# Kernel optimization log

Measured on AMD Instinct MI355X. Metric: run time of the kernel, lower is better.

Reference implementation:

```python
import jax, jax.numpy as jnp
import numpy as np

B, S, R, A, DW, DR = 64, 32, 128, 64, 512, 512

def setup_inputs() -> dict:
    key = jax.random.key(0)
    ks = jax.random.split(key, 12)
    s = 0.02
    return {
        "b_question_vector": jax.random.normal(ks[0], (B, S, DW), jnp.float32),
        "b_question_mask": jnp.zeros((B, S), dtype=bool),  # True = padding
        "b_r_space": jax.random.randint(ks[1], (B, A), 0, R),
        "b_coverage_t": jax.random.uniform(ks[2], (B, S), jnp.float32),
        "rel_emb": jax.random.normal(ks[3], (R, DR), jnp.float32) * s,
        "Wq": jax.random.normal(ks[4], (DR, DW), jnp.float32) * s,
        "bq": jnp.zeros((DR,), jnp.float32),
        "Wr": jax.random.normal(ks[5], (DR, DR), jnp.float32) * s,
        "br": jnp.zeros((DR,), jnp.float32),
        "Wc": jax.random.normal(ks[6], (DR, 1), jnp.float32) * s,
        "bc": jnp.zeros((DR,), jnp.float32),
        "Watt": jax.random.normal(ks[7], (1, DR), jnp.float32) * s,
        "batt": jnp.zeros((1,), jnp.float32),
    }

def reference(b_question_vector, b_question_mask, b_r_space, b_coverage_t,
              rel_emb, Wq, bq, Wr, br, Wc, bc, Watt, batt):
    # question_linear: [B,S,DW] -> [B,S,DR] (computed once, not repeated R times)
    qp = jnp.einsum('bsw,dw->bsd', b_question_vector, Wq) + bq
    # relation_linear over full embedding table: [R,DR]
    rp = rel_emb @ Wr.T + br
    # coverage_linear: Linear(1, DR) applied to scalar coverage -> [B,S,DR]
    cp = b_coverage_t[:, :, None] * Wc[:, 0] + bc
    # additive attention features, broadcast instead of repeat+view: [B,R,S,DR]
    feat = jnp.tanh(qp[:, None, :, :] + rp[None, :, None, :] + cp[:, None, :, :])
    # W_att: [B,R,S,DR] -> [B,R,S]
    scores = jnp.einsum('brsd,d->brs', feat, Watt[0]) + batt[0]
    scores = jnp.where(b_question_mask[:, None, :], -jnp.inf, scores)
    alpha = jax.nn.softmax(scores, axis=-1)                      # softmax over seq
    ctx = jnp.einsum('brs,bsw->brw', alpha, b_question_vector)   # [B,R,DW]
    # per-batch gather output_i[relation_i] (vectorized)
    out = jnp.take_along_axis(ctx, b_r_space[:, :, None], axis=1)    # [B,A,DW]
    alpha_sel = jnp.take_along_axis(alpha, b_r_space[:, :, None], axis=1)  # [B,A,S]
    return (out, alpha_sel)
```

## Files before the change

kernel.cpp:

```cpp
#include <hip/hip_runtime.h>
#include <hip/hip_bf16.h>
#include <math.h>

#define B_  64
#define S_  32
#define R_  128
#define A_  64
#define DW_ 512
#define DR_ 512

typedef __attribute__((ext_vector_type(8))) short short8;
typedef __attribute__((ext_vector_type(4))) float f32x4;

__device__ __forceinline__ unsigned short bf16_rn(float x) {
    union { float f; unsigned u; } v; v.f = x;
    unsigned r = v.u + 0x7FFF + ((v.u >> 16) & 1);
    return (unsigned short)(r >> 16);
}
__device__ __forceinline__ float bf16_to_f(unsigned short h) {
    union { unsigned u; float f; } v; v.u = ((unsigned)h) << 16;
    return v.f;
}

__device__ __forceinline__ int swz(int row, int chunk) {
    return row * 32 + ((chunk ^ ((row >> 1) & 3)) << 3);
}

__global__ __launch_bounds__(256) void gemm_dual_kernel(
    const float* __restrict__ A0, const float* __restrict__ B0, float* __restrict__ C0,
    int M0, int N0, int K0,
    const float* __restrict__ bias1_0, const float* __restrict__ bias2_0,
    const float* __restrict__ rowv0, const float* __restrict__ colv0,
    const float* __restrict__ A1, const float* __restrict__ B1, float* __restrict__ C1,
    int M1, int N1, int K1,
    const float* __restrict__ bias1_1)
{
    const int z = blockIdx.z;
    const float* Am; const float* Bm; float* C;
    const float *bias1, *bias2, *rowv, *colv;
    int M, N, K;
    if (z == 0) {
        Am = A0; Bm = B0; C = C0; M = M0; N = N0; K = K0;
        bias1 = bias1_0; bias2 = bias2_0; rowv = rowv0; colv = colv0;
    } else {
        Am = A1; Bm = B1; C = C1; M = M1; N = N1; K = K1;
        bias1 = bias1_1; bias2 = nullptr; rowv = nullptr; colv = nullptr;
    }

    const int bm = blockIdx.x * 64;
    const int bn = blockIdx.y * 64;
    if (bm >= M || bn >= N) return;

    __shared__ unsigned short Ahi[2][64 * 32], Alo[2][64 * 32];
    __shared__ unsigned short Bhi[2][64 * 32], Blo[2][64 * 32];

    const int tid  = threadIdx.x;
    const int l    = tid & 63;
    const int w    = tid >> 6;
    const int wr   = w >> 1;
    const int wc   = w & 1;
    const int fr   = l & 15;
    const int fc   = l >> 4;
    const int srow = tid >> 2;
    const int sch  = tid & 3;

    f32x4 acc[2][2] = {};

    float4 ra0, ra1, rb0, rb1;

    {
        const size_t arow = (size_t)(bm + srow) * K + sch * 8;
        const size_t brow = (size_t)(bn + srow) * K + sch * 8;
        ra0 = *(const float4*)&Am[arow];     ra1 = *(const float4*)&Am[arow + 4];
        rb0 = *(const float4*)&Bm[brow];     rb1 = *(const float4*)&Bm[brow + 4];

        short8 ahi, alo, bhi, blo;
        float af[8] = {ra0.x, ra0.y, ra0.z, ra0.w, ra1.x, ra1.y, ra1.z, ra1.w};
        float bf[8] = {rb0.x, rb0.y, rb0.z, rb0.w, rb1.x, rb1.y, rb1.z, rb1.w};
        #pragma unroll
        for (int e = 0; e < 8; ++e) {
            unsigned short h = bf16_rn(af[e]);
            ahi[e] = (short)h;
            alo[e] = (short)bf16_rn(af[e] - bf16_to_f(h));
            unsigned short g = bf16_rn(bf[e]);
            bhi[e] = (short)g;
            blo[e] = (short)bf16_rn(bf[e] - bf16_to_f(g));
        }
        *(short8*)&Ahi[0][swz(srow, sch)] = ahi;
        *(short8*)&Alo[0][swz(srow, sch)] = alo;
        *(short8*)&Bhi[0][swz(srow, sch)] = bhi;
        *(short8*)&Blo[0][swz(srow, sch)] = blo;
    }
    __syncthreads();

    const int nsteps = K >> 5;
    int cur = 0;
    for (int s = 0; s < nsteps; ++s) {
        if (s + 1 < nsteps) {
            const int k0 = (s + 1) << 5;
            const size_t arow = (size_t)(bm + srow) * K + k0 + sch * 8;
            const size_t brow = (size_t)(bn + srow) * K + k0 + sch * 8;
            ra0 = *(const float4*)&Am[arow];     ra1 = *(const float4*)&Am[arow + 4];
            rb0 = *(const float4*)&Bm[brow];     rb1 = *(const float4*)&Bm[brow + 4];
        }

        short8 fahi[2], falo[2], fbhi[2], fblo[2];
        #pragma unroll
        for (int i = 0; i < 2; ++i) {
            const int r = wr * 32 + i * 16 + fr;
            fahi[i] = *(const short8*)&Ahi[cur][swz(r, fc)];
            falo[i] = *(const short8*)&Alo[cur][swz(r, fc)];
            const int c = wc * 32 + i * 16 + fr;
            fbhi[i] = *(const short8*)&Bhi[cur][swz(c, fc)];
            fblo[i] = *(const short8*)&Blo[cur][swz(c, fc)];
        }
        #pragma unroll
        for (int i = 0; i < 2; ++i)
            #pragma unroll
            for (int j = 0; j < 2; ++j) {
                acc[i][j] = __builtin_amdgcn_mfma_f32_16x16x32_bf16(fahi[i], fbhi[j], acc[i][j], 0, 0, 0);
                acc[i][j] = __builtin_amdgcn_mfma_f32_16x16x32_bf16(fahi[i], fblo[j], acc[i][j], 0, 0, 0);
                acc[i][j] = __builtin_amdgcn_mfma_f32_16x16x32_bf16(falo[i], fbhi[j], acc[i][j], 0, 0, 0);
            }

        if (s + 1 < nsteps) {
            short8 ahi, alo, bhi, blo;
            float af[8] = {ra0.x, ra0.y, ra0.z, ra0.w, ra1.x, ra1.y, ra1.z, ra1.w};
            float bf[8] = {rb0.x, rb0.y, rb0.z, rb0.w, rb1.x, rb1.y, rb1.z, rb1.w};
            #pragma unroll
            for (int e = 0; e < 8; ++e) {
                unsigned short h = bf16_rn(af[e]);
                ahi[e] = (short)h;
                alo[e] = (short)bf16_rn(af[e] - bf16_to_f(h));
                unsigned short g = bf16_rn(bf[e]);
                bhi[e] = (short)g;
                blo[e] = (short)bf16_rn(bf[e] - bf16_to_f(g));
            }
            const int nxt = cur ^ 1;
            *(short8*)&Ahi[nxt][swz(srow, sch)] = ahi;
            *(short8*)&Alo[nxt][swz(srow, sch)] = alo;
            *(short8*)&Bhi[nxt][swz(srow, sch)] = bhi;
            *(short8*)&Blo[nxt][swz(srow, sch)] = blo;
            __syncthreads();
            cur = nxt;
        }
    }

    #pragma unroll
    for (int i = 0; i < 2; ++i)
        #pragma unroll
        for (int j = 0; j < 2; ++j) {
            const int n  = bn + wc * 32 + j * 16 + fr;
            const float b1 = bias1[n];
            const float b2 = bias2 ? bias2[n] : 0.0f;
            const float cv = colv ? colv[n] : 0.0f;
            #pragma unroll
            for (int reg = 0; reg < 4; ++reg) {
                const int m = bm + wr * 32 + i * 16 + fc * 4 + reg;
                float v = acc[i][j][reg] + b1 + b2;
                if (rowv) v += rowv[m] * cv;
                C[(size_t)m * N + n] = v;
            }
        }
}

__global__ __launch_bounds__(256) void attn_kernel(
    const float* __restrict__ u,
    const float* __restrict__ rp,
    const float* __restrict__ watt,
    const float* __restrict__ battp,
    const float* __restrict__ qv,
    const unsigned char* __restrict__ mask,
    const int* __restrict__ rspace,
    float* __restrict__ out,
    float* __restrict__ alpha_out)
{
    const int blk  = blockIdx.x;
    const int b    = blk >> 3;
    const int ba0  = b * A_ + ((blk & 7) << 3);
    const int tid  = threadIdx.x;
    const int lane = tid & 63;
    const int wave = tid >> 6;

    const float K2 = 2.8853900817779268f;

    __shared__ float s_scores[8][S_];
    __shared__ float s_alpha[8][S_];

    float wav[8], rp2[8][8];
    {
        const float4* wa4 = (const float4*)watt;
        #pragma unroll
        for (int v = 0; v < 2; ++v) {
            float4 w = wa4[v * 64 + lane];
            wav[v*4+0] = w.x; wav[v*4+1] = w.y; wav[v*4+2] = w.z; wav[v*4+3] = w.w;
        }
        #pragma unroll
        for (int g = 0; g < 8; ++g) {
            const float4* rp4 = (const float4*)(rp + (size_t)rspace[ba0 + g] * DR_);
            #pragma unroll
            for (int v = 0; v < 2; ++v) {
                float4 t = rp4[v * 64 + lane];
                rp2[g][v*4+0] = t.x * K2; rp2[g][v*4+1] = t.y * K2;
                rp2[g][v*4+2] = t.z * K2; rp2[g][v*4+3] = t.w * K2;
            }
        }
    }
    const float batt = battp[0];

    float swa = wav[0] + wav[1] + wav[2] + wav[3] + wav[4] + wav[5] + wav[6] + wav[7];
    #pragma unroll
    for (int off = 32; off > 0; off >>= 1)
        swa += __shfl_xor(swa, off);

    #pragma unroll
    for (int si = 0; si < 8; ++si) {
        const int s = (wave << 3) + si;
        const float4* u4 = (const float4*)(u + ((size_t)b * S_ + s) * DR_);
        float uu[8];
        #pragma unroll
        for (int v = 0; v < 2; ++v) {
            float4 t = u4[v * 64 + lane];
            uu[v*4+0] = t.x; uu[v*4+1] = t.y; uu[v*4+2] = t.z; uu[v*4+3] = t.w;
        }
        float ac[8] = {};
        #pragma unroll
        for (int e = 0; e < 8; ++e) {
            const float ue = uu[e];
            const float we = wav[e];
            const float uk = ue * K2;
            #pragma unroll
            for (int g = 0; g < 8; ++g) {
                float zz = __builtin_amdgcn_exp2f(uk + rp2[g][e]);
                ac[g] = fmaf(we, __builtin_amdgcn_rcpf(zz + 1.0f), ac[g]);
            }
        }
        #pragma unroll
        for (int off = 32; off > 0; off >>= 1)
            #pragma unroll
            for (int g = 0; g < 8; ++g)
                ac[g] += __shfl_xor(ac[g], off);
        if (lane == 0)
            #pragma unroll
            for (int g = 0; g < 8; ++g)
                s_scores[g][s] = fmaf(-2.0f, ac[g], swa) + batt;
    }
    __syncthreads();

    {
        const int g = tid >> 5;
        const int s = tid & 31;
        float sc = s_scores[g][s];
        if (mask[b * S_ + s]) sc = -INFINITY;
        float m = sc;
        #pragma unroll
        for (int off = 16; off > 0; off >>= 1)
            m = fmaxf(m, __shfl_xor(m, off));
        float e = __expf(sc - m);
        float sum = e;
        #pragma unroll
        for (int off = 16; off > 0; off >>= 1)
            sum += __shfl_xor(sum, off);
        float al = e / sum;
        s_alpha[g][s] = al;
        alpha_out[(size_t)(ba0 + g) * S_ + s] = al;
    }
    __syncthreads();

    float2 acc2[8] = {};
    const float* qb = qv + (size_t)b * S_ * DW_;
    #pragma unroll 4
    for (int s = 0; s < S_; ++s) {
        float2 q = *(const float2*)&qb[s * DW_ + tid * 2];
        #pragma unroll
        for (int g = 0; g < 8; ++g) {
            const float al = s_alpha[g][s];
            acc2[g].x = fmaf(al, q.x, acc2[g].x);
            acc2[g].y = fmaf(al, q.y, acc2[g].y);
        }
    }
    #pragma unroll
    for (int g = 0; g < 8; ++g)
        *(float2*)&out[(size_t)(ba0 + g) * DW_ + tid * 2] = acc2[g];
}

extern "C" void kernel_launch(void* const* d_in, const int* in_sizes, int n_in,
                              void* d_out, int out_size, void* d_ws, size_t ws_size,
                              hipStream_t stream) {
    const float*         qv   = (const float*)d_in[0];
    const unsigned char* mask = (const unsigned char*)d_in[1];
    const int*           rsp  = (const int*)d_in[2];
    const float*         cov  = (const float*)d_in[3];
    const float*         rel  = (const float*)d_in[4];
    const float*         Wq   = (const float*)d_in[5];
    const float*         bq   = (const float*)d_in[6];
    const float*         Wr   = (const float*)d_in[7];
    const float*         br   = (const float*)d_in[8];
    const float*         Wc   = (const float*)d_in[9];
    const float*         bc   = (const float*)d_in[10];
    const float*         Watt = (const float*)d_in[11];
    const float*         batt = (const float*)d_in[12];

    float* u  = (float*)d_ws;
    float* rp = u + (size_t)B_ * S_ * DR_;

    float* out       = (float*)d_out;
    float* alpha_out = out + (size_t)B_ * A_ * DW_;

    dim3 blk(256);

    gemm_dual_kernel<<<dim3((B_ * S_) / 64, DR_ / 64, 2), blk, 0, stream>>>(
        qv, Wq, u, B_ * S_, DR_, DW_, bq, bc, cov, Wc,
        rel, Wr, rp, R_, DR_, DR_, br);

    attn_kernel<<<dim3(B_ * (A_ / 8)), blk, 0, stream>>>(
        u, rp, Watt, batt, qv, mask, rsp, out, alpha_out);
}
```

Before: 120.7 us.

## Pre-split GEMM operands into swizzled bf16 hi/lo tiles in a prep kernel

Adds a prep kernel that converts qv, Wq, rel_emb and Wr into bf16 hi/lo pairs, pre-swizzled and tiled so the GEMM can copy each tile straight into LDS with no conversion work. The GEMM tile drops to 32x64 to double the block count, and the main loop now only moves short8 data. This takes the split-conversion arithmetic out of the GEMM loop and shrinks its load traffic. In exchange it adds a kernel launch and a workspace write and read of the packed data, and the weights are converted again on every call.

Result: no change. 121.2 us (+0.4%).

```diff
diff --git a/kernel.cpp b/kernel.cpp
--- a/kernel.cpp
+++ b/kernel.cpp
@@ -11,13 +11,14 @@
 
 typedef __attribute__((ext_vector_type(8))) short short8;
 typedef __attribute__((ext_vector_type(4))) float f32x4;
-
-__device__ __forceinline__ unsigned short bf16_rn(float x) {
+typedef unsigned short ushort_t;
+
+__device__ __forceinline__ ushort_t bf16_rn(float x) {
     union { float f; unsigned u; } v; v.f = x;
     unsigned r = v.u + 0x7FFF + ((v.u >> 16) & 1);
-    return (unsigned short)(r >> 16);
-}
-__device__ __forceinline__ float bf16_to_f(unsigned short h) {
+    return (ushort_t)(r >> 16);
+}
+__device__ __forceinline__ float bf16_to_f(ushort_t h) {
     union { unsigned u; float f; } v; v.u = ((unsigned)h) << 16;
     return v.f;
 }
@@ -26,142 +27,142 @@
     return row * 32 + ((chunk ^ ((row >> 1) & 3)) << 3);
 }
 
-__global__ __launch_bounds__(256) void gemm_dual_kernel(
-    const float* __restrict__ A0, const float* __restrict__ B0, float* __restrict__ C0,
-    int M0, int N0, int K0,
+__global__ __launch_bounds__(256) void prep_kernel(
+    const float* __restrict__ qv, const float* __restrict__ Wq,
+    const float* __restrict__ rel, const float* __restrict__ Wr,
+    ushort_t* __restrict__ pk_qv, ushort_t* __restrict__ pk_Wq,
+    ushort_t* __restrict__ pk_rel, ushort_t* __restrict__ pk_Wr)
+{
+    const int gid = blockIdx.x * 256 + threadIdx.x;
+    const float* X; ushort_t* P; int lid, trs;
+    if (gid < 131072)      { X = qv;  P = pk_qv;  lid = gid;          trs = 5; }
+    else if (gid < 163840) { X = Wq;  P = pk_Wq;  lid = gid - 131072; trs = 6; }
+    else if (gid < 172032) { X = rel; P = pk_rel; lid = gid - 163840; trs = 5; }
+    else                   { X = Wr;  P = pk_Wr;  lid = gid - 172032; trs = 6; }
+
+    const int row  = lid >> 6;
+    const int c8   = lid & 63;
+    const int ks   = c8 >> 2;
+    const int sch  = c8 & 3;
+    const int rblk = row >> trs;
+    const int srow = row & ((1 << trs) - 1);
+    const int tsz  = 32 << trs;
+
+    const float* src = X + (size_t)row * 512 + ks * 32 + sch * 8;
+    float4 v0 = *(const float4*)src;
+    float4 v1 = *(const float4*)(src + 4);
+    float f[8] = {v0.x, v0.y, v0.z, v0.w, v1.x, v1.y, v1.z, v1.w};
+    short8 hi, lo;
+    #pragma unroll
+    for (int e = 0; e < 8; ++e) {
+        ushort_t h = bf16_rn(f[e]);
+        hi[e] = (short)h;
+        lo[e] = (short)bf16_rn(f[e] - bf16_to_f(h));
+    }
+    const size_t base = (size_t)(rblk * 16 + ks) * (size_t)(tsz * 2);
+    *(short8*)&P[base + swz(srow, sch)]       = hi;
+    *(short8*)&P[base + tsz + swz(srow, sch)] = lo;
+}
+
+__global__ __launch_bounds__(256) void gemm_pk_kernel(
+    const ushort_t* __restrict__ pkA0, const ushort_t* __restrict__ pkB0,
+    float* __restrict__ C0, int M0, int N0,
     const float* __restrict__ bias1_0, const float* __restrict__ bias2_0,
     const float* __restrict__ rowv0, const float* __restrict__ colv0,
-    const float* __restrict__ A1, const float* __restrict__ B1, float* __restrict__ C1,
-    int M1, int N1, int K1,
+    const ushort_t* __restrict__ pkA1, const ushort_t* __restrict__ pkB1,
+    float* __restrict__ C1, int M1, int N1,
     const float* __restrict__ bias1_1)
 {
     const int z = blockIdx.z;
-    const float* Am; const float* Bm; float* C;
+    const ushort_t* pkA; const ushort_t* pkB; float* C;
     const float *bias1, *bias2, *rowv, *colv;
-    int M, N, K;
+    int M, N;
     if (z == 0) {
-        Am = A0; Bm = B0; C = C0; M = M0; N = N0; K = K0;
+        pkA = pkA0; pkB = pkB0; C = C0; M = M0; N = N0;
         bias1 = bias1_0; bias2 = bias2_0; rowv = rowv0; colv = colv0;
     } else {
-        Am = A1; Bm = B1; C = C1; M = M1; N = N1; K = K1;
+        pkA = pkA1; pkB = pkB1; C = C1; M = M1; N = N1;
         bias1 = bias1_1; bias2 = nullptr; rowv = nullptr; colv = nullptr;
     }
 
-    const int bm = blockIdx.x * 64;
+    const int bm = blockIdx.x * 32;
     const int bn = blockIdx.y * 64;
     if (bm >= M || bn >= N) return;
 
-    __shared__ unsigned short Ahi[2][64 * 32], Alo[2][64 * 32];
-    __shared__ unsigned short Bhi[2][64 * 32], Blo[2][64 * 32];
-
-    const int tid  = threadIdx.x;
-    const int l    = tid & 63;
-    const int w    = tid >> 6;
-    const int wr   = w >> 1;
-    const int wc   = w & 1;
-    const int fr   = l & 15;
-    const int fc   = l >> 4;
-    const int srow = tid >> 2;
-    const int sch  = tid & 3;
-
-    f32x4 acc[2][2] = {};
-
-    float4 ra0, ra1, rb0, rb1;
+    __shared__ ushort_t Ab[2][2048];
+    __shared__ ushort_t Bb[2][4096];
+
+    const int tid = threadIdx.x;
+    const int l   = tid & 63;
+    const int w   = tid >> 6;
+    const int wr  = w >> 1;
+    const int wc  = w & 1;
+    const int fr  = l & 15;
+    const int fc  = l >> 4;
+
+    f32x4 acc[2] = {};
+
+    const size_t tA = (size_t)blockIdx.x * 16;
+    const size_t tB = (size_t)blockIdx.y * 16;
 
     {
-        const size_t arow = (size_t)(bm + srow) * K + sch * 8;
-        const size_t brow = (size_t)(bn + srow) * K + sch * 8;
-        ra0 = *(const float4*)&Am[arow];     ra1 = *(const float4*)&Am[arow + 4];
-        rb0 = *(const float4*)&Bm[brow];     rb1 = *(const float4*)&Bm[brow + 4];
-
-        short8 ahi, alo, bhi, blo;
-        float af[8] = {ra0.x, ra0.y, ra0.z, ra0.w, ra1.x, ra1.y, ra1.z, ra1.w};
-        float bf[8] = {rb0.x, rb0.y, rb0.z, rb0.w, rb1.x, rb1.y, rb1.z, rb1.w};
-        #pragma unroll
-        for (int e = 0; e < 8; ++e) {
-            unsigned short h = bf16_rn(af[e]);
-            ahi[e] = (short)h;
-            alo[e] = (short)bf16_rn(af[e] - bf16_to_f(h));
-            unsigned short g = bf16_rn(bf[e]);
-            bhi[e] = (short)g;
-            blo[e] = (short)bf16_rn(bf[e] - bf16_to_f(g));
-        }
-        *(short8*)&Ahi[0][swz(srow, sch)] = ahi;
-        *(short8*)&Alo[0][swz(srow, sch)] = alo;
-        *(short8*)&Bhi[0][swz(srow, sch)] = bhi;
-        *(short8*)&Blo[0][swz(srow, sch)] = blo;
+        const ushort_t* sA = pkA + (tA << 11);
+        const ushort_t* sB = pkB + (tB << 12);
+        *(short8*)&Ab[0][tid << 3]          = *(const short8*)&sA[tid << 3];
+        *(short8*)&Bb[0][tid << 3]          = *(const short8*)&sB[tid << 3];
+        *(short8*)&Bb[0][(tid << 3) + 2048] = *(const short8*)&sB[(tid << 3) + 2048];
     }
     __syncthreads();
 
-    const int nsteps = K >> 5;
     int cur = 0;
-    for (int s = 0; s < nsteps; ++s) {
-        if (s + 1 < nsteps) {
-            const int k0 = (s + 1) << 5;
-            const size_t arow = (size_t)(bm + srow) * K + k0 + sch * 8;
-            const size_t brow = (size_t)(bn + srow) * K + k0 + sch * 8;
-            ra0 = *(const float4*)&Am[arow];     ra1 = *(const float4*)&Am[arow + 4];
-            rb0 = *(const float4*)&Bm[brow];     rb1 = *(const float4*)&Bm[brow + 4];
-        }
-
-        short8 fahi[2], falo[2], fbhi[2], fblo[2];
-        #pragma unroll
-        for (int i = 0; i < 2; ++i) {
-            const int r = wr * 32 + i * 16 + fr;
-            fahi[i] = *(const short8*)&Ahi[cur][swz(r, fc)];
-            falo[i] = *(const short8*)&Alo[cur][swz(r, fc)];
-            const int c = wc * 32 + i * 16 + fr;
-            fbhi[i] = *(const short8*)&Bhi[cur][swz(c, fc)];
-            fblo[i] = *(const short8*)&Blo[cur][swz(c, fc)];
-        }
-        #pragma unroll
-        for (int i = 0; i < 2; ++i)
-            #pragma unroll
-            for (int j = 0; j < 2; ++j) {
-                acc[i][j] = __builtin_amdgcn_mfma_f32_16x16x32_bf16(fahi[i], fbhi[j], acc[i][j], 0, 0, 0);
-                acc[i][j] = __builtin_amdgcn_mfma_f32_16x16x32_bf16(fahi[i], fblo[j], acc[i][j], 0, 0, 0);
-                acc[i][j] = __builtin_amdgcn_mfma_f32_16x16x32_bf16(falo[i], fbhi[j], acc[i][j], 0, 0, 0);
-            }
-
-        if (s + 1 < nsteps) {
-            short8 ahi, alo, bhi, blo;
-            float af[8] = {ra0.x, ra0.y, ra0.z, ra0.w, ra1.x, ra1.y, ra1.z, ra1.w};
-            float bf[8] = {rb0.x, rb0.y, rb0.z, rb0.w, rb1.x, rb1.y, rb1.z, rb1.w};
-            #pragma unroll
-            for (int e = 0; e < 8; ++e) {
-                unsigned short h = bf16_rn(af[e]);
-                ahi[e] = (short)h;
-                alo[e] = (short)bf16_rn(af[e] - bf16_to_f(h));
-                unsigned short g = bf16_rn(bf[e]);
-                bhi[e] = (short)g;
-                blo[e] = (short)bf16_rn(bf[e] - bf16_to_f(g));
-            }
+    #pragma unroll 4
+    for (int s = 0; s < 16; ++s) {
+        short8 la, lb0, lb1;
+        if (s + 1 < 16) {
+            const ushort_t* sA = pkA + ((tA + s + 1) << 11);
+            const ushort_t* sB = pkB + ((tB + s + 1) << 12);
+            la  = *(const short8*)&sA[tid << 3];
+            lb0 = *(const short8*)&sB[tid << 3];
+            lb1 = *(const short8*)&sB[(tid << 3) + 2048];
+        }
+
+        const int ra = wr * 16 + fr;
+        short8 ahi = *(const short8*)&Ab[cur][swz(ra, fc)];
+        short8 alo = *(const short8*)&Ab[cur][1024 + swz(ra, fc)];
+        #pragma unroll
+        for (int j = 0; j < 2; ++j) {
+            const int c = wc * 32 + j * 16 + fr;
+            short8 bhi = *(const short8*)&Bb[cur][swz(c, fc)];
+            short8 blo = *(const short8*)&Bb[cur][2048 + swz(c, fc)];
+            acc[j] = __builtin_amdgcn_mfma_f32_16x16x32_bf16(ahi, bhi, acc[j], 0, 0, 0);
+            acc[j] = __builtin_amdgcn_mfma_f32_16x16x32_bf16(ahi, blo, acc[j], 0, 0, 0);
+            acc[j] = __builtin_amdgcn_mfma_f32_16x16x32_bf16(alo, bhi, acc[j], 0, 0, 0);
+        }
+
+        if (s + 1 < 16) {
             const int nxt = cur ^ 1;
-            *(short8*)&Ahi[nxt][swz(srow, sch)] = ahi;
-            *(short8*)&Alo[nxt][swz(srow, sch)] = alo;
-            *(short8*)&Bhi[nxt][swz(srow, sch)] = bhi;
-            *(short8*)&Blo[nxt][swz(srow, sch)] = blo;
+            *(short8*)&Ab[nxt][tid << 3]          = la;
+            *(short8*)&Bb[nxt][tid << 3]          = lb0;
+            *(short8*)&Bb[nxt][(tid << 3) + 2048] = lb1;
             __syncthreads();
             cur = nxt;
         }
     }
 
     #pragma unroll
-    for (int i = 0; i < 2; ++i)
-        #pragma unroll
-        for (int j = 0; j < 2; ++j) {
-            const int n  = bn + wc * 32 + j * 16 + fr;
-            const float b1 = bias1[n];
-            const float b2 = bias2 ? bias2[n] : 0.0f;
-            const float cv = colv ? colv[n] : 0.0f;
-            #pragma unroll
-            for (int reg = 0; reg < 4; ++reg) {
-                const int m = bm + wr * 32 + i * 16 + fc * 4 + reg;
-                float v = acc[i][j][reg] + b1 + b2;
-                if (rowv) v += rowv[m] * cv;
-                C[(size_t)m * N + n] = v;
-            }
-        }
+    for (int j = 0; j < 2; ++j) {
+        const int n  = bn + wc * 32 + j * 16 + fr;
+        const float b1 = bias1[n];
+        const float b2 = bias2 ? bias2[n] : 0.0f;
+        const float cv = colv ? colv[n] : 0.0f;
+        #pragma unroll
+        for (int reg = 0; reg < 4; ++reg) {
+            const int m = bm + wr * 16 + fc * 4 + reg;
+            float v = acc[j][reg] + b1 + b2;
+            if (rowv) v += rowv[m] * cv;
+            C[(size_t)m * N + n] = v;
+        }
+    }
 }
 
 __global__ __launch_bounds__(256) void attn_kernel(
@@ -226,9 +227,8 @@
         float ac[8] = {};
         #pragma unroll
         for (int e = 0; e < 8; ++e) {
-            const float ue = uu[e];
             const float we = wav[e];
-            const float uk = ue * K2;
+            const float uk = uu[e] * K2;
             #pragma unroll
             for (int g = 0; g < 8; ++g) {
                 float zz = __builtin_amdgcn_exp2f(uk + rp2[g][e]);
@@ -301,17 +301,25 @@
     const float*         Watt = (const float*)d_in[11];
     const float*         batt = (const float*)d_in[12];
 
-    float* u  = (float*)d_ws;
-    float* rp = u + (size_t)B_ * S_ * DR_;
+    float*    u      = (float*)d_ws;
+    float*    rp     = u + (size_t)B_ * S_ * DR_;
+    ushort_t* pk     = (ushort_t*)(rp + (size_t)R_ * DR_);
+    ushort_t* pk_qv  = pk;
+    ushort_t* pk_Wq  = pk_qv  + 2097152;
+    ushort_t* pk_rel = pk_Wq  + 524288;
+    ushort_t* pk_Wr  = pk_rel + 131072;
 
     float* out       = (float*)d_out;
     float* alpha_out = out + (size_t)B_ * A_ * DW_;
 
     dim3 blk(256);
 
-    gemm_dual_kernel<<<dim3((B_ * S_) / 64, DR_ / 64, 2), blk, 0, stream>>>(
-        qv, Wq, u, B_ * S_, DR_, DW_, bq, bc, cov, Wc,
-        rel, Wr, rp, R_, DR_, DR_, br);
+    prep_kernel<<<dim3(800), blk, 0, stream>>>(
+        qv, Wq, rel, Wr, pk_qv, pk_Wq, pk_rel, pk_Wr);
+
+    gemm_pk_kernel<<<dim3(64, 8, 2), blk, 0, stream>>>(
+        pk_qv, pk_Wq, u, B_ * S_, DR_, bq, bc, cov, Wc,
+        pk_rel, pk_Wr, rp, R_, DR_, br);
 
     attn_kernel<<<dim3(B_ * (A_ / 8)), blk, 0, stream>>>(
         u, rp, Watt, batt, qv, mask, rsp, out, alpha_out);
```
